# Performance work log

Hardware: AMD Instinct MI355X
Metric: run time of the kernel (lower is better)

## Reference

```python
import jax, jax.numpy as jnp
import numpy as np

EPS = 1e-5

def setup_inputs() -> dict:
    key = jax.random.key(0)
    ks = jax.random.split(key, 6)
    N, E, C, H, L = 50000, 800000, 128, 128, 3
    x = jax.random.normal(ks[0], (N, C), dtype=jnp.float32)
    edge_index = jax.random.randint(ks[1], (2, E), 0, N, dtype=jnp.int64)
    # Xavier-ish scaled weights; layer 0 uses in=C=H so all layers stack uniformly.
    Wl = jax.random.normal(ks[2], (L, C, H), dtype=jnp.float32) / np.sqrt(C)
    Wr = jax.random.normal(ks[3], (L, C, H), dtype=jnp.float32) / np.sqrt(C)
    b = jnp.zeros((L, H), dtype=jnp.float32)
    gamma = jnp.ones((L, H), dtype=jnp.float32)
    beta = jnp.zeros((L, H), dtype=jnp.float32)
    return {"x": x, "edge_index": edge_index, "Wl": Wl, "Wr": Wr, "b": b,
            "gamma": gamma, "beta": beta}

def _sage_bn_relu(x, src, dst, Wl, Wr, b, gamma, beta):
    N = x.shape[0]
    # mean aggregation of source features into target nodes (PyG SAGEConv default)
    agg = jax.ops.segment_sum(x[src], dst, num_segments=N)          # [N, C]
    deg = jax.ops.segment_sum(jnp.ones_like(dst, dtype=x.dtype), dst, num_segments=N)
    mean_nbr = agg / jnp.maximum(deg, 1.0)[:, None]
    h = mean_nbr @ Wl + x @ Wr + b                                   # [N, H]
    # BatchNorm1d (training-mode batch statistics over nodes)
    mu = jnp.mean(h, axis=0)
    var = jnp.var(h, axis=0)
    h = gamma * (h - mu) * jax.lax.rsqrt(var + EPS) + beta
    return jax.nn.relu(h)  # dropout omitted (deterministic reference, p->0)

def reference(x, edge_index, Wl, Wr, b, gamma, beta):
    src, dst = edge_index[0], edge_index[1]
    h = x
    for l in range(Wl.shape[0]):
        h = _sage_bn_relu(h, src, dst, Wl[l], Wr[l], b[l], gamma[l], beta[l])
    return h
```

## Files before the change

kernel.cpp:

```cpp
#include <hip/hip_runtime.h>
#include <hip/hip_bf16.h>

#define BN_EPS 1e-5f
#define BCAP 16384

typedef unsigned short u16;
typedef unsigned int u32;
typedef __attribute__((ext_vector_type(8))) short bf16x8v;
typedef __attribute__((ext_vector_type(4))) float f32x4v;

__device__ __forceinline__ float bf2f(u16 u){
    union { u32 i; float f; } c; c.i = ((u32)u) << 16; return c.f;
}
__device__ __forceinline__ u16 f2bf(float f){
    union { float f; u32 i; } c; c.f = f;
    u32 x = c.i;
    u32 r = x + 0x7FFFu + ((x >> 16) & 1u);
    return (u16)(r >> 16);
}
__device__ __forceinline__ float lo16(u32 u){
    union { u32 i; float f; } c; c.i = u << 16; return c.f;
}
__device__ __forceinline__ float hi16(u32 u){
    union { u32 i; float f; } c; c.i = u & 0xFFFF0000u; return c.f;
}
__device__ __forceinline__ u32 pack2(float f0, float f1){
    return (u32)f2bf(f0) | ((u32)f2bf(f1) << 16);
}

__global__ void detect_k(const int* __restrict__ ei, const u16* __restrict__ xu,
                         int* __restrict__ flags){
    int lane = threadIdx.x;
    unsigned long long bal = __ballot(ei[2 * lane + 1] != 0);
    int cnt = 0;
    #pragma unroll
    for (int k = 0; k < 4; ++k){
        u16 u = xu[2 * (lane + 64 * k)];
        int e = (u >> 7) & 0xFF;
        cnt += (e >= 0x70 && e <= 0x86) ? 1 : 0;
    }
    #pragma unroll
    for (int off = 1; off < 64; off <<= 1) cnt += __shfl_xor(cnt, off);
    if (lane == 0){
        flags[0] = (bal == 0ULL) ? 1 : 0;
        flags[1] = (cnt >= 128) ? 1 : 0;
    }
}

__global__ void prep_k(const void* __restrict__ x, const void* __restrict__ Wl,
                       const void* __restrict__ Wr, const void* __restrict__ b,
                       const void* __restrict__ g, const void* __restrict__ be,
                       u16* __restrict__ xb, u16* __restrict__ wT, float* __restrict__ p,
                       int total4, int wtot, int per, const int* __restrict__ flags){
    int i = blockIdx.x * blockDim.x + threadIdx.x;
    int bf = flags[1];
    if (i < total4){
        if (bf){
            ((uint2*)xb)[i] = ((const uint2*)x)[i];
        } else {
            float4 v = ((const float4*)x)[i];
            ushort4 o; o.x = f2bf(v.x); o.y = f2bf(v.y); o.z = f2bf(v.z); o.w = f2bf(v.w);
            ((ushort4*)xb)[i] = o;
        }
    }
    if (i < wtot){
        u16 vl = bf ? ((const u16*)Wl)[i] : f2bf(((const float*)Wl)[i]);
        u16 vr = bf ? ((const u16*)Wr)[i] : f2bf(((const float*)Wr)[i]);
        int l = i >> 14, r = (i >> 7) & 127, c = i & 127;
        wT[(size_t)(l * 2 + 0) * 16384 + c * 128 + r] = vl;
        wT[(size_t)(l * 2 + 1) * 16384 + c * 128 + r] = vr;
    }
    if (i < per){
        if (bf){
            p[i]           = bf2f(((const u16*)b)[i]);
            p[per + i]     = bf2f(((const u16*)g)[i]);
            p[2 * per + i] = bf2f(((const u16*)be)[i]);
        } else {
            p[i]           = ((const float*)b)[i];
            p[per + i]     = ((const float*)g)[i];
            p[2 * per + i] = ((const float*)be)[i];
        }
    }
}

__global__ __launch_bounds__(1024) void phist_k(const void* __restrict__ ei, int E,
                                                int tile, u32* __restrict__ blockHist,
                                                const int* __restrict__ flags){
    __shared__ u32 lh[128];
    int tid = threadIdx.x;
    if (tid < 128) lh[tid] = 0u;
    __syncthreads();
    int start = blockIdx.x * tile;
    int end = min(E, start + tile);
    int i64 = flags[0];
    for (int i = start + tid; i < end; i += 1024){
        int d = i64 ? (int)((const long long*)ei)[E + i] : ((const int*)ei)[E + i];
        atomicAdd(&lh[d >> 9], 1u);
    }
    __syncthreads();
    if (tid < 128) blockHist[blockIdx.x * 128 + tid] = lh[tid];
}

__global__ void bases_k(const u32* __restrict__ blockHist, u32* __restrict__ blockBase,
                        int* __restrict__ rangeBase, int* __restrict__ rowptrN, int nb){
    __shared__ u32 t_s[128];
    int k = threadIdx.x;
    u32 run = 0;
    for (int b = 0; b < nb; ++b){
        blockBase[b * 128 + k] = run;
        run += blockHist[b * 128 + k];
    }
    t_s[k] = min(run, (u32)BCAP);
    __syncthreads();
    if (k == 0){
        u32 r = 0;
        for (int j = 0; j < 128; ++j){ u32 v = t_s[j]; t_s[j] = r; r += v; }
        rangeBase[128] = (int)r;
        *rowptrN = (int)r;
    }
    __syncthreads();
    rangeBase[k] = (int)t_s[k];
}

__global__ __launch_bounds__(1024) void pscat_k(const void* __restrict__ ei, int E,
                                                int tile, const u32* __restrict__ blockBase,
                                                u32* __restrict__ part,
                                                const int* __restrict__ flags){
    __shared__ u32 lcur[128];
    int tid = threadIdx.x;
    if (tid < 128) lcur[tid] = blockBase[blockIdx.x * 128 + tid];
    __syncthreads();
    int start = blockIdx.x * tile;
    int end = min(E, start + tile);
    int i64 = flags[0];
    for (int i = start + tid; i < end; i += 1024){
        int s, d;
        if (i64){
            const long long* p = (const long long*)ei;
            s = (int)p[i]; d = (int)p[E + i];
        } else {
            const int* p = (const int*)ei;
            s = p[i]; d = p[E + i];
        }
        int k = d >> 9;
        u32 pos = atomicAdd(&lcur[k], 1u);
        if (pos < BCAP) part[(size_t)k * BCAP + pos] = (u32)(u16)s | ((u32)(d & 511) << 16);
    }
}

__global__ __launch_bounds__(1024) void build_k(const u32* __restrict__ part,
                                                const int* __restrict__ rangeBase,
                                                int* __restrict__ rowptr,
                                                float* __restrict__ dinv,
                                                u16* __restrict__ col, int N){
    __shared__ u32 bins[512];
    __shared__ u32 wsum[8];
    __shared__ u16 sorted[BCAP];
    int k   = blockIdx.x;
    int tid = threadIdx.x;
    int base = rangeBase[k];
    int cntk = rangeBase[k + 1] - base;
    int d0   = k << 9;
    if (tid < 512) bins[tid] = 0u;
    __syncthreads();
    const u32* pk = part + (size_t)k * BCAP;
    for (int i = tid; i < cntk; i += 1024)
        atomicAdd(&bins[pk[i] >> 16], 1u);
    __syncthreads();
    int lane = tid & 63, w = tid >> 6;
    u32 v = (tid < 512) ? bins[tid] : 0u;
    u32 sc = v;
    #pragma unroll
    for (int off = 1; off < 64; off <<= 1){
        u32 u = __shfl_up(sc, off);
        if (lane >= off) sc += u;
    }
    if (lane == 63 && w < 8) wsum[w] = sc;
    __syncthreads();
    if (tid == 0){
        u32 r = 0;
        #pragma unroll
        for (int j = 0; j < 8; ++j){ u32 t = wsum[j]; wsum[j] = r; r += t; }
    }
    __syncthreads();
    u32 excl = (w < 8 ? wsum[w] : 0u) + sc - v;
    if (tid < 512){
        int d = d0 + tid;
        if (d < N){
            rowptr[d] = base + (int)excl;
            dinv[d] = 1.f / fmaxf((float)v, 1.f);
        }
        bins[tid] = excl;
    }
    __syncthreads();
    for (int i = tid; i < cntk; i += 1024){
        u32 e = pk[i];
        u32 pos = atomicAdd(&bins[e >> 16], 1u);
        sorted[pos] = (u16)e;
    }
    __syncthreads();
    for (int i = tid; i < cntk; i += 1024)
        col[base + i] = sorted[i];
}

__global__ void agg_k(const u16* __restrict__ h, const int* __restrict__ rowptr,
                      const u16* __restrict__ col, const float* __restrict__ dinv,
                      u16* __restrict__ meanb, int N){
    int wid  = (blockIdx.x * blockDim.x + threadIdx.x) >> 6;
    int lane = threadIdx.x & 63;
    if (wid >= N) return;
    int q   = lane >> 4;
    int sub = lane & 15;
    int s = rowptr[wid], e = rowptr[wid + 1];
    float a[8] = {0.f,0.f,0.f,0.f,0.f,0.f,0.f,0.f};
    int i = s + q;
    for (; i + 4 < e; i += 8){
        int sn0 = col[i], sn1 = col[i + 4];
        uint4 v0 = *(const uint4*)(h + (size_t)sn0 * 128 + sub * 8);
        uint4 v1 = *(const uint4*)(h + (size_t)sn1 * 128 + sub * 8);
        a[0] += lo16(v0.x) + lo16(v1.x); a[1] += hi16(v0.x) + hi16(v1.x);
        a[2] += lo16(v0.y) + lo16(v1.y); a[3] += hi16(v0.y) + hi16(v1.y);
        a[4] += lo16(v0.z) + lo16(v1.z); a[5] += hi16(v0.z) + hi16(v1.z);
        a[6] += lo16(v0.w) + lo16(v1.w); a[7] += hi16(v0.w) + hi16(v1.w);
    }
    if (i < e){
        int sn = col[i];
        uint4 v = *(const uint4*)(h + (size_t)sn * 128 + sub * 8);
        a[0] += lo16(v.x); a[1] += hi16(v.x);
        a[2] += lo16(v.y); a[3] += hi16(v.y);
        a[4] += lo16(v.z); a[5] += hi16(v.z);
        a[6] += lo16(v.w); a[7] += hi16(v.w);
    }
    #pragma unroll
    for (int off = 16; off < 64; off <<= 1){
        #pragma unroll
        for (int j = 0; j < 8; ++j) a[j] += __shfl_xor(a[j], off);
    }
    if (q == 0){
        float di = dinv[wid];
        uint4 o;
        o.x = pack2(a[0] * di, a[1] * di);
        o.y = pack2(a[2] * di, a[3] * di);
        o.z = pack2(a[4] * di, a[5] * di);
        o.w = pack2(a[6] * di, a[7] * di);
        *(uint4*)(meanb + (size_t)wid * 128 + sub * 8) = o;
    }
}

__global__ __launch_bounds__(256) void gemm_k(
        const u16* __restrict__ Aa, const u16* __restrict__ Ab,
        const u16* __restrict__ wT, const float* __restrict__ bias,
        u16* __restrict__ hp16, float* __restrict__ stats, int N){
    __shared__ float s_stat[256];
    int tid  = threadIdx.x;
    int lane = tid & 63;
    int w    = tid >> 6;
    int wid  = blockIdx.x * 4 + w;
    int hl   = lane & 15;
    int quad = lane >> 4;
    int m0   = wid * 32;
    s_stat[tid] = 0.f;
    __syncthreads();

    f32x4v acc[2][8];
    #pragma unroll
    for (int r2 = 0; r2 < 2; ++r2)
        #pragma unroll
        for (int t = 0; t < 8; ++t) acc[r2][t] = (f32x4v){0.f, 0.f, 0.f, 0.f};

    if (m0 < N){
        const u16* arow0[2];
        const u16* arow1[2];
        #pragma unroll
        for (int r2 = 0; r2 < 2; ++r2){
            int rb = m0 + r2 * 16;
            if (rb + 16 > N) rb = N - 16;
            arow0[r2] = Aa + (size_t)(rb + hl) * 128 + quad * 8;
            arow1[r2] = Ab + (size_t)(rb + hl) * 128 + quad * 8;
        }
        #pragma unroll
        for (int half = 0; half < 2; ++half){
            const u16* A0 = half ? arow1[0] : arow0[0];
            const u16* A1 = half ? arow1[1] : arow0[1];
            const u16* Bp = wT + half * 16384 + (size_t)hl * 128 + quad * 8;
            #pragma unroll
            for (int kc = 0; kc < 128; kc += 32){
                bf16x8v af0 = *(const bf16x8v*)(A0 + kc);
                bf16x8v af1 = *(const bf16x8v*)(A1 + kc);
                #pragma unroll
                for (int t = 0; t < 8; ++t){
                    bf16x8v bf = *(const bf16x8v*)(Bp + t * 2048 + kc);
                    acc[0][t] = __builtin_amdgcn_mfma_f32_16x16x32_bf16(af0, bf, acc[0][t], 0, 0, 0);
                    acc[1][t] = __builtin_amdgcn_mfma_f32_16x16x32_bf16(af1, bf, acc[1][t], 0, 0, 0);
                }
            }
        }
    }

    #pragma unroll
    for (int r2 = 0; r2 < 2; ++r2){
        int mb = m0 + r2 * 16;
        bool valid = (mb < N);
        #pragma unroll
        for (int t = 0; t < 8; ++t){
            int c = t * 16 + hl;
            float bv = bias[c];
            float cs = 0.f, cq = 0.f;
            if (valid){
                #pragma unroll
                for (int r = 0; r < 4; ++r){
                    float v = acc[r2][t][r] + bv;
                    hp16[(size_t)(mb + quad * 4 + r) * 128 + c] = f2bf(v);
                    cs += v; cq += v * v;
                }
            }
            cs += __shfl_xor(cs, 16); cs += __shfl_xor(cs, 32);
            cq += __shfl_xor(cq, 16); cq += __shfl_xor(cq, 32);
            if (quad == 0 && valid){
                atomicAdd(&s_stat[c], cs);
                atomicAdd(&s_stat[128 + c], cq);
            }
        }
    }
    __syncthreads();
    float* st = stats + (size_t)(blockIdx.x & 63) * 256;
    atomicAdd(&st[tid], s_stat[tid]);
}

__global__ void finalize_k(float* __restrict__ stats, const float* __restrict__ g,
                           const float* __restrict__ be, float* __restrict__ ss, float invN){
    int j = threadIdx.x;
    float s = 0.f, sq = 0.f;
    #pragma unroll 8
    for (int bkt = 0; bkt < 64; ++bkt){
        s  += stats[bkt * 256 + j];
        sq += stats[bkt * 256 + 128 + j];
        stats[bkt * 256 + j] = 0.f;
        stats[bkt * 256 + 128 + j] = 0.f;
    }
    float mu  = s * invN;
    float var = sq * invN - mu * mu;
    if (!(mu == mu)) mu = 0.f;
    if (!(var >= 0.f) || !(var == var)) var = 0.f;
    float sc = g[j] * rsqrtf(var + BN_EPS);
    ss[j]       = sc;
    ss[128 + j] = be[j] - mu * sc;
}

__global__ void apply_k(const u16* __restrict__ in, const float* __restrict__ ss,
                        u16* __restrict__ outb, float* __restrict__ outf, int use_f32,
                        int total4){
    int i = blockIdx.x * blockDim.x + threadIdx.x;
    if (i >= total4) return;
    uint2 u = ((const uint2*)in)[i];
    float4 v;
    v.x = lo16(u.x); v.y = hi16(u.x); v.z = lo16(u.y); v.w = hi16(u.y);
    if (!(v.x == v.x)) v.x = 0.f;
    if (!(v.y == v.y)) v.y = 0.f;
    if (!(v.z == v.z)) v.z = 0.f;
    if (!(v.w == v.w)) v.w = 0.f;
    int c = (i & 31) * 4;
    float r0 = fmaxf(v.x * ss[c]     + ss[128 + c], 0.f);
    float r1 = fmaxf(v.y * ss[c + 1] + ss[129 + c], 0.f);
    float r2 = fmaxf(v.z * ss[c + 2] + ss[130 + c], 0.f);
    float r3 = fmaxf(v.w * ss[c + 3] + ss[131 + c], 0.f);
    if (use_f32){
        float4 o; o.x = r0; o.y = r1; o.z = r2; o.w = r3;
        ((float4*)outf)[i] = o;
    } else {
        uint2 o; o.x = pack2(r0, r1); o.y = pack2(r2, r3);
        ((uint2*)outb)[i] = o;
    }
}

extern "C" void kernel_launch(void* const* d_in, const int* in_sizes, int n_in,
                              void* d_out, int out_size, void* d_ws, size_t ws_size,
                              hipStream_t stream){
    const void* x  = d_in[0];
    const int*  ei = (const int*)d_in[1];
    const void* Wl = d_in[2];
    const void* Wr = d_in[3];
    const void* b  = d_in[4];
    const void* gm = d_in[5];
    const void* bt = d_in[6];
    float* outf = (float*)d_out;

    const int N = in_sizes[0] / 128;
    const int E = in_sizes[1] / 2;
    const int L = in_sizes[2] / 16384;
    const int PB = 128;
    const int TILE = (E + PB - 1) / PB;

    char* wsp = (char*)d_ws;
    size_t off = 0;
    auto alloc = [&](size_t bytes) -> char* {
        char* p = wsp + off;
        off = (off + bytes + 255) & ~(size_t)255;
        return p;
    };
    int*   flags  = (int*)  alloc(16);
    int*   rowptr = (int*)  alloc((size_t)(N + 1) * 4);
    u16*   col    = (u16*)  alloc((size_t)E * 2);
    float* dinv   = (float*)alloc((size_t)N * 4);
    u32*   bHist  = (u32*)  alloc((size_t)PB * 128 * 4);
    u32*   bBase  = (u32*)  alloc((size_t)PB * 128 * 4);
    int*   rangeB = (int*)  alloc((size_t)129 * 4);
    u32*   part   = (u32*)  alloc((size_t)128 * BCAP * 4);
    u16*   wT     = (u16*)  alloc((size_t)L * 2 * 16384 * 2);
    float* pvec   = (float*)alloc((size_t)3 * L * 128 * 4);
    float* ss     = (float*)alloc(256 * 4);
    u16*   xb     = (u16*)  alloc((size_t)N * 128 * 2);
    u16*   meanb  = (u16*)  alloc((size_t)N * 128 * 2);
    float* stats  = (float*)alloc((size_t)64 * 256 * 4);
    u16*   hpre16 = (u16*)  alloc((size_t)N * 128 * 2);
    u16*   hA     = (u16*)  alloc((size_t)N * 128 * 2);
    u16*   hB     = (u16*)  alloc((size_t)N * 128 * 2);
    (void)ws_size; (void)n_in; (void)out_size;

    detect_k<<<1, 64, 0, stream>>>(ei, (const u16*)x, flags);
    hipMemsetAsync(stats, 0, (size_t)64 * 256 * 4, stream);

    phist_k<<<PB, 1024, 0, stream>>>((const void*)ei, E, TILE, bHist, flags);
    bases_k<<<1, 128, 0, stream>>>(bHist, bBase, rangeB, rowptr + N, PB);
    pscat_k<<<PB, 1024, 0, stream>>>((const void*)ei, E, TILE, bBase, part, flags);
    build_k<<<128, 1024, 0, stream>>>(part, rangeB, rowptr, dinv, col, N);

    prep_k<<<(N * 32 + 255) / 256, 256, 0, stream>>>(x, Wl, Wr, b, gm, bt, xb, wT, pvec,
                                                     N * 32, L * 16384, L * 128, flags);

    const u16* state = xb;
    int nwaves = (N + 31) / 32;
    int gblocks = (nwaves + 3) / 4;
    for (int l = 0; l < L; ++l){
        int last = (l == L - 1);
        u16* nxt = (l & 1) ? hB : hA;
        agg_k<<<(N + 3) / 4, 256, 0, stream>>>(state, rowptr, col, dinv, meanb, N);
        gemm_k<<<gblocks, 256, 0, stream>>>(meanb, state, wT + (size_t)l * 2 * 16384,
                                            pvec + l * 128, hpre16, stats, N);
        finalize_k<<<1, 128, 0, stream>>>(stats, pvec + (size_t)L * 128 + l * 128,
                                          pvec + (size_t)2 * L * 128 + l * 128,
                                          ss, 1.f / (float)N);
        apply_k<<<(N * 32 + 255) / 256, 256, 0, stream>>>(hpre16, ss, nxt, outf, last,
                                                          N * 32);
        state = nxt;
    }
}
```

Before: 350.4 us.

## Fuse GEMM, BatchNorm finalize and apply via in-kernel grid barrier

The GEMM kernel now keeps its pre-norm outputs in registers, accumulates batch statistics, and waits on a software grid-wide barrier. After the barrier every block computes the scale and shift and writes the normalized ReLU output directly. This removes the finalize and apply launches and the bf16 round trip of the intermediate activation. The catch is that it depends on all 196 blocks of 512 threads being resident at once, and it contends on a single global stats array instead of 64 buckets; the spin loop has a timeout that would silently give wrong results if residency fails.

After: 394.5 us. 1.13x slower.

```diff
diff --git a/kernel.cpp b/kernel.cpp
--- a/kernel.cpp
+++ b/kernel.cpp
@@ -247,19 +247,23 @@
     }
 }
 
-__global__ __launch_bounds__(256) void gemm_k(
+__global__ __launch_bounds__(512, 2) void gemm_k(
         const u16* __restrict__ Aa, const u16* __restrict__ Ab,
         const u16* __restrict__ wT, const float* __restrict__ bias,
-        u16* __restrict__ hp16, float* __restrict__ stats, int N){
+        const float* __restrict__ gamma, const float* __restrict__ beta,
+        float* __restrict__ stats, u32* __restrict__ bar,
+        u16* __restrict__ outb, float* __restrict__ outf,
+        int use_f32, int N, float invN){
     __shared__ float s_stat[256];
+    __shared__ float s_ss[256];
     int tid  = threadIdx.x;
     int lane = tid & 63;
     int w    = tid >> 6;
-    int wid  = blockIdx.x * 4 + w;
+    int wid  = blockIdx.x * 8 + w;
     int hl   = lane & 15;
     int quad = lane >> 4;
     int m0   = wid * 32;
-    s_stat[tid] = 0.f;
+    if (tid < 256) s_stat[tid] = 0.f;
     __syncthreads();
 
     f32x4v acc[2][8];
@@ -295,81 +299,85 @@
                 }
             }
         }
-    }
-
-    #pragma unroll
-    for (int r2 = 0; r2 < 2; ++r2){
-        int mb = m0 + r2 * 16;
-        bool valid = (mb < N);
-        #pragma unroll
-        for (int t = 0; t < 8; ++t){
-            int c = t * 16 + hl;
-            float bv = bias[c];
-            float cs = 0.f, cq = 0.f;
-            if (valid){
+
+        #pragma unroll
+        for (int r2 = 0; r2 < 2; ++r2){
+            int mb = m0 + r2 * 16;
+            bool valid = (mb < N);
+            #pragma unroll
+            for (int t = 0; t < 8; ++t){
+                int c = t * 16 + hl;
+                float bv = bias[c];
+                float cs = 0.f, cq = 0.f;
                 #pragma unroll
                 for (int r = 0; r < 4; ++r){
                     float v = acc[r2][t][r] + bv;
-                    hp16[(size_t)(mb + quad * 4 + r) * 128 + c] = f2bf(v);
+                    acc[r2][t][r] = v;
                     cs += v; cq += v * v;
                 }
+                cs += __shfl_xor(cs, 16); cs += __shfl_xor(cs, 32);
+                cq += __shfl_xor(cq, 16); cq += __shfl_xor(cq, 32);
+                if (quad == 0 && valid){
+                    atomicAdd(&s_stat[c], cs);
+                    atomicAdd(&s_stat[128 + c], cq);
+                }
             }
-            cs += __shfl_xor(cs, 16); cs += __shfl_xor(cs, 32);
-            cq += __shfl_xor(cq, 16); cq += __shfl_xor(cq, 32);
-            if (quad == 0 && valid){
-                atomicAdd(&s_stat[c], cs);
-                atomicAdd(&s_stat[128 + c], cq);
+        }
+    }
+    __syncthreads();
+    if (tid < 256) atomicAdd(&stats[tid], s_stat[tid]);
+
+    __syncthreads();
+    if (tid == 0){
+        __threadfence();
+        u32 nb = gridDim.x;
+        u32 my = __hip_atomic_load(&bar[1], __ATOMIC_RELAXED, __HIP_MEMORY_SCOPE_AGENT);
+        u32 old = __hip_atomic_fetch_add(&bar[0], 1u, __ATOMIC_ACQ_REL, __HIP_MEMORY_SCOPE_AGENT);
+        if (old == nb - 1){
+            __hip_atomic_store(&bar[0], 0u, __ATOMIC_RELAXED, __HIP_MEMORY_SCOPE_AGENT);
+            __hip_atomic_fetch_add(&bar[1], 1u, __ATOMIC_RELEASE, __HIP_MEMORY_SCOPE_AGENT);
+        } else {
+            int spins = 0;
+            while (__hip_atomic_load(&bar[1], __ATOMIC_ACQUIRE, __HIP_MEMORY_SCOPE_AGENT) == my){
+                __builtin_amdgcn_s_sleep(2);
+                if (++spins > 20000000) break;
             }
         }
     }
     __syncthreads();
-    float* st = stats + (size_t)(blockIdx.x & 63) * 256;
-    atomicAdd(&st[tid], s_stat[tid]);
-}
-
-__global__ void finalize_k(float* __restrict__ stats, const float* __restrict__ g,
-                           const float* __restrict__ be, float* __restrict__ ss, float invN){
-    int j = threadIdx.x;
-    float s = 0.f, sq = 0.f;
-    #pragma unroll 8
-    for (int bkt = 0; bkt < 64; ++bkt){
-        s  += stats[bkt * 256 + j];
-        sq += stats[bkt * 256 + 128 + j];
-        stats[bkt * 256 + j] = 0.f;
-        stats[bkt * 256 + 128 + j] = 0.f;
-    }
-    float mu  = s * invN;
-    float var = sq * invN - mu * mu;
-    if (!(mu == mu)) mu = 0.f;
-    if (!(var >= 0.f) || !(var == var)) var = 0.f;
-    float sc = g[j] * rsqrtf(var + BN_EPS);
-    ss[j]       = sc;
-    ss[128 + j] = be[j] - mu * sc;
-}
-
-__global__ void apply_k(const u16* __restrict__ in, const float* __restrict__ ss,
-                        u16* __restrict__ outb, float* __restrict__ outf, int use_f32,
-                        int total4){
-    int i = blockIdx.x * blockDim.x + threadIdx.x;
-    if (i >= total4) return;
-    uint2 u = ((const uint2*)in)[i];
-    float4 v;
-    v.x = lo16(u.x); v.y = hi16(u.x); v.z = lo16(u.y); v.w = hi16(u.y);
-    if (!(v.x == v.x)) v.x = 0.f;
-    if (!(v.y == v.y)) v.y = 0.f;
-    if (!(v.z == v.z)) v.z = 0.f;
-    if (!(v.w == v.w)) v.w = 0.f;
-    int c = (i & 31) * 4;
-    float r0 = fmaxf(v.x * ss[c]     + ss[128 + c], 0.f);
-    float r1 = fmaxf(v.y * ss[c + 1] + ss[129 + c], 0.f);
-    float r2 = fmaxf(v.z * ss[c + 2] + ss[130 + c], 0.f);
-    float r3 = fmaxf(v.w * ss[c + 3] + ss[131 + c], 0.f);
-    if (use_f32){
-        float4 o; o.x = r0; o.y = r1; o.z = r2; o.w = r3;
-        ((float4*)outf)[i] = o;
-    } else {
-        uint2 o; o.x = pack2(r0, r1); o.y = pack2(r2, r3);
-        ((uint2*)outb)[i] = o;
+
+    if (tid < 128){
+        float s  = __hip_atomic_load(&stats[tid],       __ATOMIC_RELAXED, __HIP_MEMORY_SCOPE_AGENT);
+        float sq = __hip_atomic_load(&stats[128 + tid], __ATOMIC_RELAXED, __HIP_MEMORY_SCOPE_AGENT);
+        float mu  = s * invN;
+        float var = sq * invN - mu * mu;
+        if (!(mu == mu)) mu = 0.f;
+        if (!(var >= 0.f) || !(var == var)) var = 0.f;
+        float sc = gamma[tid] * rsqrtf(var + BN_EPS);
+        s_ss[tid]       = sc;
+        s_ss[128 + tid] = beta[tid] - mu * sc;
+    }
+    __syncthreads();
+
+    if (m0 < N){
+        #pragma unroll
+        for (int r2 = 0; r2 < 2; ++r2){
+            int mb = m0 + r2 * 16;
+            if (mb >= N) continue;
+            #pragma unroll
+            for (int t = 0; t < 8; ++t){
+                int c = t * 16 + hl;
+                float sc = s_ss[c];
+                float sh = s_ss[128 + c];
+                #pragma unroll
+                for (int r = 0; r < 4; ++r){
+                    float y = fmaxf(acc[r2][t][r] * sc + sh, 0.f);
+                    size_t idx = (size_t)(mb + quad * 4 + r) * 128 + c;
+                    if (use_f32) outf[idx] = y;
+                    else         outb[idx] = f2bf(y);
+                }
+            }
+        }
     }
 }
 
@@ -408,17 +416,16 @@
     u32*   part   = (u32*)  alloc((size_t)128 * BCAP * 4);
     u16*   wT     = (u16*)  alloc((size_t)L * 2 * 16384 * 2);
     float* pvec   = (float*)alloc((size_t)3 * L * 128 * 4);
-    float* ss     = (float*)alloc(256 * 4);
+    u32*   bar    = (u32*)  alloc(256);
+    float* stats  = (float*)alloc((size_t)L * 256 * 4);
     u16*   xb     = (u16*)  alloc((size_t)N * 128 * 2);
     u16*   meanb  = (u16*)  alloc((size_t)N * 128 * 2);
-    float* stats  = (float*)alloc((size_t)64 * 256 * 4);
-    u16*   hpre16 = (u16*)  alloc((size_t)N * 128 * 2);
     u16*   hA     = (u16*)  alloc((size_t)N * 128 * 2);
     u16*   hB     = (u16*)  alloc((size_t)N * 128 * 2);
     (void)ws_size; (void)n_in; (void)out_size;
 
     detect_k<<<1, 64, 0, stream>>>(ei, (const u16*)x, flags);
-    hipMemsetAsync(stats, 0, (size_t)64 * 256 * 4, stream);
+    hipMemsetAsync(bar, 0, 256 + (size_t)L * 256 * 4, stream);
 
     phist_k<<<PB, 1024, 0, stream>>>((const void*)ei, E, TILE, bHist, flags);
     bases_k<<<1, 128, 0, stream>>>(bHist, bBase, rangeB, rowptr + N, PB);
@@ -429,19 +436,19 @@
                                                      N * 32, L * 16384, L * 128, flags);
 
     const u16* state = xb;
-    int nwaves = (N + 31) / 32;
-    int gblocks = (nwaves + 3) / 4;
+    int nwaves  = (N + 31) / 32;
+    int gblocks = (nwaves + 7) / 8;
+    float invN  = 1.f / (float)N;
     for (int l = 0; l < L; ++l){
         int last = (l == L - 1);
         u16* nxt = (l & 1) ? hB : hA;
         agg_k<<<(N + 3) / 4, 256, 0, stream>>>(state, rowptr, col, dinv, meanb, N);
-        gemm_k<<<gblocks, 256, 0, stream>>>(meanb, state, wT + (size_t)l * 2 * 16384,
-                                            pvec + l * 128, hpre16, stats, N);
-        finalize_k<<<1, 128, 0, stream>>>(stats, pvec + (size_t)L * 128 + l * 128,
-                                          pvec + (size_t)2 * L * 128 + l * 128,
-                                          ss, 1.f / (float)N);
-        apply_k<<<(N * 32 + 255) / 256, 256, 0, stream>>>(hpre16, ss, nxt, outf, last,
-                                                          N * 32);
+        gemm_k<<<gblocks, 512, 0, stream>>>(meanb, state, wT + (size_t)l * 2 * 16384,
+                                            pvec + (size_t)l * 128,
+                                            pvec + (size_t)L * 128 + (size_t)l * 128,
+                                            pvec + (size_t)2 * L * 128 + (size_t)l * 128,
+                                            stats + (size_t)l * 256, bar,
+                                            nxt, outf, last, N, invN);
         state = nxt;
     }
 }
```

## Fold BatchNorm+ReLU of previous layer into next layer's aggregation and GEMM loads

Applied to the files above, without the earlier changes.

Drops the per-layer apply pass. The raw pre-activation output of each layer is stored as the state, and the previous layer's BN scale/shift plus ReLU are applied on the fly. This happens when neighbor features are gathered in agg_k and when the self features are loaded in gemm_k. A single apply_k runs only at the end to write the fp32 output. The GEMM also moves from 32 to 16 rows per wave. Per-layer stats buffers remove the zeroing inside finalize. Each edge gather now pays an extra FMA and max per element, and the GEMM does per-element bf16 conversion on the self operand; in exchange, two full-tensor passes per layer go away.

Result: slower. 383.4 us (+9.4%).

```diff
diff --git a/kernel.cpp b/kernel.cpp
--- a/kernel.cpp
+++ b/kernel.cpp
@@ -51,6 +51,7 @@
                        const void* __restrict__ Wr, const void* __restrict__ b,
                        const void* __restrict__ g, const void* __restrict__ be,
                        u16* __restrict__ xb, u16* __restrict__ wT, float* __restrict__ p,
+                       float* __restrict__ ssAll,
                        int total4, int wtot, int per, const int* __restrict__ flags){
     int i = blockIdx.x * blockDim.x + threadIdx.x;
     int bf = flags[1];
@@ -80,6 +81,10 @@
             p[per + i]     = ((const float*)g)[i];
             p[2 * per + i] = ((const float*)be)[i];
         }
+    }
+    if (i < 128){
+        ssAll[i]       = 1.f;
+        ssAll[128 + i] = 0.f;
     }
 }
 
@@ -205,32 +210,45 @@
 
 __global__ void agg_k(const u16* __restrict__ h, const int* __restrict__ rowptr,
                       const u16* __restrict__ col, const float* __restrict__ dinv,
-                      u16* __restrict__ meanb, int N){
+                      const float* __restrict__ ss, u16* __restrict__ meanb,
+                      float reluLo, int N){
     int wid  = (blockIdx.x * blockDim.x + threadIdx.x) >> 6;
     int lane = threadIdx.x & 63;
     if (wid >= N) return;
     int q   = lane >> 4;
     int sub = lane & 15;
+    float scr[8], shr[8];
+    #pragma unroll
+    for (int j = 0; j < 8; ++j){
+        scr[j] = ss[sub * 8 + j];
+        shr[j] = ss[128 + sub * 8 + j];
+    }
     int s = rowptr[wid], e = rowptr[wid + 1];
     float a[8] = {0.f,0.f,0.f,0.f,0.f,0.f,0.f,0.f};
     int i = s + q;
+    #define BNR(x, j) fmaxf((x) * scr[j] + shr[j], reluLo)
     for (; i + 4 < e; i += 8){
         int sn0 = col[i], sn1 = col[i + 4];
         uint4 v0 = *(const uint4*)(h + (size_t)sn0 * 128 + sub * 8);
         uint4 v1 = *(const uint4*)(h + (size_t)sn1 * 128 + sub * 8);
-        a[0] += lo16(v0.x) + lo16(v1.x); a[1] += hi16(v0.x) + hi16(v1.x);
-        a[2] += lo16(v0.y) + lo16(v1.y); a[3] += hi16(v0.y) + hi16(v1.y);
-        a[4] += lo16(v0.z) + lo16(v1.z); a[5] += hi16(v0.z) + hi16(v1.z);
-        a[6] += lo16(v0.w) + lo16(v1.w); a[7] += hi16(v0.w) + hi16(v1.w);
+        a[0] += BNR(lo16(v0.x),0) + BNR(lo16(v1.x),0);
+        a[1] += BNR(hi16(v0.x),1) + BNR(hi16(v1.x),1);
+        a[2] += BNR(lo16(v0.y),2) + BNR(lo16(v1.y),2);
+        a[3] += BNR(hi16(v0.y),3) + BNR(hi16(v1.y),3);
+        a[4] += BNR(lo16(v0.z),4) + BNR(lo16(v1.z),4);
+        a[5] += BNR(hi16(v0.z),5) + BNR(hi16(v1.z),5);
+        a[6] += BNR(lo16(v0.w),6) + BNR(lo16(v1.w),6);
+        a[7] += BNR(hi16(v0.w),7) + BNR(hi16(v1.w),7);
     }
     if (i < e){
         int sn = col[i];
         uint4 v = *(const uint4*)(h + (size_t)sn * 128 + sub * 8);
-        a[0] += lo16(v.x); a[1] += hi16(v.x);
-        a[2] += lo16(v.y); a[3] += hi16(v.y);
-        a[4] += lo16(v.z); a[5] += hi16(v.z);
-        a[6] += lo16(v.w); a[7] += hi16(v.w);
-    }
+        a[0] += BNR(lo16(v.x),0); a[1] += BNR(hi16(v.x),1);
+        a[2] += BNR(lo16(v.y),2); a[3] += BNR(hi16(v.y),3);
+        a[4] += BNR(lo16(v.z),4); a[5] += BNR(hi16(v.z),5);
+        a[6] += BNR(lo16(v.w),6); a[7] += BNR(hi16(v.w),7);
+    }
+    #undef BNR
     #pragma unroll
     for (int off = 16; off < 64; off <<= 1){
         #pragma unroll
@@ -250,73 +268,74 @@
 __global__ __launch_bounds__(256) void gemm_k(
         const u16* __restrict__ Aa, const u16* __restrict__ Ab,
         const u16* __restrict__ wT, const float* __restrict__ bias,
-        u16* __restrict__ hp16, float* __restrict__ stats, int N){
+        const float* __restrict__ ssPrev, float* __restrict__ stats,
+        u16* __restrict__ hp16, float reluLo, int N){
     __shared__ float s_stat[256];
+    __shared__ float s_ss[256];
     int tid  = threadIdx.x;
     int lane = tid & 63;
     int w    = tid >> 6;
     int wid  = blockIdx.x * 4 + w;
     int hl   = lane & 15;
     int quad = lane >> 4;
-    int m0   = wid * 32;
+    int m0   = wid * 16;
     s_stat[tid] = 0.f;
-    __syncthreads();
-
-    f32x4v acc[2][8];
-    #pragma unroll
-    for (int r2 = 0; r2 < 2; ++r2)
+    s_ss[tid]   = ssPrev[tid];
+    __syncthreads();
+
+    f32x4v acc[8];
+    #pragma unroll
+    for (int t = 0; t < 8; ++t) acc[t] = (f32x4v){0.f, 0.f, 0.f, 0.f};
+
+    if (m0 < N){
+        int rb = m0;
+        if (rb + 16 > N) rb = N - 16;
+        const u16* a0 = Aa + (size_t)(rb + hl) * 128 + quad * 8;
+        const u16* a1 = Ab + (size_t)(rb + hl) * 128 + quad * 8;
+
         #pragma unroll
-        for (int t = 0; t < 8; ++t) acc[r2][t] = (f32x4v){0.f, 0.f, 0.f, 0.f};
-
-    if (m0 < N){
-        const u16* arow0[2];
-        const u16* arow1[2];
+        for (int kc = 0; kc < 128; kc += 32){
+            bf16x8v af = *(const bf16x8v*)(a0 + kc);
+            const u16* Bp = wT + (size_t)hl * 128 + quad * 8 + kc;
+            #pragma unroll
+            for (int t = 0; t < 8; ++t){
+                bf16x8v bf = *(const bf16x8v*)(Bp + t * 2048);
+                acc[t] = __builtin_amdgcn_mfma_f32_16x16x32_bf16(af, bf, acc[t], 0, 0, 0);
+            }
+        }
         #pragma unroll
-        for (int r2 = 0; r2 < 2; ++r2){
-            int rb = m0 + r2 * 16;
-            if (rb + 16 > N) rb = N - 16;
-            arow0[r2] = Aa + (size_t)(rb + hl) * 128 + quad * 8;
-            arow1[r2] = Ab + (size_t)(rb + hl) * 128 + quad * 8;
-        }
-        #pragma unroll
-        for (int half = 0; half < 2; ++half){
-            const u16* A0 = half ? arow1[0] : arow0[0];
-            const u16* A1 = half ? arow1[1] : arow0[1];
-            const u16* Bp = wT + half * 16384 + (size_t)hl * 128 + quad * 8;
+        for (int kc = 0; kc < 128; kc += 32){
+            bf16x8v raw = *(const bf16x8v*)(a1 + kc);
+            bf16x8v af;
             #pragma unroll
-            for (int kc = 0; kc < 128; kc += 32){
-                bf16x8v af0 = *(const bf16x8v*)(A0 + kc);
-                bf16x8v af1 = *(const bf16x8v*)(A1 + kc);
-                #pragma unroll
-                for (int t = 0; t < 8; ++t){
-                    bf16x8v bf = *(const bf16x8v*)(Bp + t * 2048 + kc);
-                    acc[0][t] = __builtin_amdgcn_mfma_f32_16x16x32_bf16(af0, bf, acc[0][t], 0, 0, 0);
-                    acc[1][t] = __builtin_amdgcn_mfma_f32_16x16x32_bf16(af1, bf, acc[1][t], 0, 0, 0);
-                }
+            for (int j = 0; j < 8; ++j){
+                int c = quad * 8 + kc + j;
+                float f = bf2f((u16)raw[j]);
+                f = fmaxf(f * s_ss[c] + s_ss[128 + c], reluLo);
+                af[j] = (short)f2bf(f);
             }
-        }
-    }
-
-    #pragma unroll
-    for (int r2 = 0; r2 < 2; ++r2){
-        int mb = m0 + r2 * 16;
-        bool valid = (mb < N);
+            const u16* Bp = wT + 16384 + (size_t)hl * 128 + quad * 8 + kc;
+            #pragma unroll
+            for (int t = 0; t < 8; ++t){
+                bf16x8v bf = *(const bf16x8v*)(Bp + t * 2048);
+                acc[t] = __builtin_amdgcn_mfma_f32_16x16x32_bf16(af, bf, acc[t], 0, 0, 0);
+            }
+        }
+
         #pragma unroll
         for (int t = 0; t < 8; ++t){
             int c = t * 16 + hl;
             float bv = bias[c];
             float cs = 0.f, cq = 0.f;
-            if (valid){
-                #pragma unroll
-                for (int r = 0; r < 4; ++r){
-                    float v = acc[r2][t][r] + bv;
-                    hp16[(size_t)(mb + quad * 4 + r) * 128 + c] = f2bf(v);
-                    cs += v; cq += v * v;
-                }
+            #pragma unroll
+            for (int r = 0; r < 4; ++r){
+                float v = acc[t][r] + bv;
+                hp16[(size_t)(rb + quad * 4 + r) * 128 + c] = f2bf(v);
+                cs += v; cq += v * v;
             }
             cs += __shfl_xor(cs, 16); cs += __shfl_xor(cs, 32);
             cq += __shfl_xor(cq, 16); cq += __shfl_xor(cq, 32);
-            if (quad == 0 && valid){
+            if (quad == 0){
                 atomicAdd(&s_stat[c], cs);
                 atomicAdd(&s_stat[128 + c], cq);
             }
@@ -327,29 +346,27 @@
     atomicAdd(&st[tid], s_stat[tid]);
 }
 
-__global__ void finalize_k(float* __restrict__ stats, const float* __restrict__ g,
-                           const float* __restrict__ be, float* __restrict__ ss, float invN){
+__global__ void finalize_k(const float* __restrict__ stats, const float* __restrict__ g,
+                           const float* __restrict__ be, float* __restrict__ ssOut,
+                           float invN){
     int j = threadIdx.x;
     float s = 0.f, sq = 0.f;
     #pragma unroll 8
     for (int bkt = 0; bkt < 64; ++bkt){
         s  += stats[bkt * 256 + j];
         sq += stats[bkt * 256 + 128 + j];
-        stats[bkt * 256 + j] = 0.f;
-        stats[bkt * 256 + 128 + j] = 0.f;
     }
     float mu  = s * invN;
     float var = sq * invN - mu * mu;
     if (!(mu == mu)) mu = 0.f;
     if (!(var >= 0.f) || !(var == var)) var = 0.f;
     float sc = g[j] * rsqrtf(var + BN_EPS);
-    ss[j]       = sc;
-    ss[128 + j] = be[j] - mu * sc;
+    ssOut[j]       = sc;
+    ssOut[128 + j] = be[j] - mu * sc;
 }
 
 __global__ void apply_k(const u16* __restrict__ in, const float* __restrict__ ss,
-                        u16* __restrict__ outb, float* __restrict__ outf, int use_f32,
-                        int total4){
+                        float* __restrict__ outf, int total4){
     int i = blockIdx.x * blockDim.x + threadIdx.x;
     if (i >= total4) return;
     uint2 u = ((const uint2*)in)[i];
@@ -360,17 +377,12 @@
     if (!(v.z == v.z)) v.z = 0.f;
     if (!(v.w == v.w)) v.w = 0.f;
     int c = (i & 31) * 4;
-    float r0 = fmaxf(v.x * ss[c]     + ss[128 + c], 0.f);
-    float r1 = fmaxf(v.y * ss[c + 1] + ss[129 + c], 0.f);
-    float r2 = fmaxf(v.z * ss[c + 2] + ss[130 + c], 0.f);
-    float r3 = fmaxf(v.w * ss[c + 3] + ss[131 + c], 0.f);
-    if (use_f32){
-        float4 o; o.x = r0; o.y = r1; o.z = r2; o.w = r3;
-        ((float4*)outf)[i] = o;
-    } else {
-        uint2 o; o.x = pack2(r0, r1); o.y = pack2(r2, r3);
-        ((uint2*)outb)[i] = o;
-    }
+    float4 o;
+    o.x = fmaxf(v.x * ss[c]     + ss[128 + c], 0.f);
+    o.y = fmaxf(v.y * ss[c + 1] + ss[129 + c], 0.f);
+    o.z = fmaxf(v.z * ss[c + 2] + ss[130 + c], 0.f);
+    o.w = fmaxf(v.w * ss[c + 3] + ss[131 + c], 0.f);
+    ((float4*)outf)[i] = o;
 }
 
 extern "C" void kernel_launch(void* const* d_in, const int* in_sizes, int n_in,
@@ -408,17 +420,16 @@
     u32*   part   = (u32*)  alloc((size_t)128 * BCAP * 4);
     u16*   wT     = (u16*)  alloc((size_t)L * 2 * 16384 * 2);
     float* pvec   = (float*)alloc((size_t)3 * L * 128 * 4);
-    float* ss     = (float*)alloc(256 * 4);
+    float* ssAll  = (float*)alloc((size_t)(L + 1) * 256 * 4);
+    float* stats  = (float*)alloc((size_t)L * 64 * 256 * 4);
     u16*   xb     = (u16*)  alloc((size_t)N * 128 * 2);
     u16*   meanb  = (u16*)  alloc((size_t)N * 128 * 2);
-    float* stats  = (float*)alloc((size_t)64 * 256 * 4);
-    u16*   hpre16 = (u16*)  alloc((size_t)N * 128 * 2);
     u16*   hA     = (u16*)  alloc((size_t)N * 128 * 2);
     u16*   hB     = (u16*)  alloc((size_t)N * 128 * 2);
     (void)ws_size; (void)n_in; (void)out_size;
 
     detect_k<<<1, 64, 0, stream>>>(ei, (const u16*)x, flags);
-    hipMemsetAsync(stats, 0, (size_t)64 * 256 * 4, stream);
+    hipMemsetAsync(stats, 0, (size_t)L * 64 * 256 * 4, stream);
 
     phist_k<<<PB, 1024, 0, stream>>>((const void*)ei, E, TILE, bHist, flags);
     bases_k<<<1, 128, 0, stream>>>(bHist, bBase, rangeB, rowptr + N, PB);
@@ -426,22 +437,29 @@
     build_k<<<128, 1024, 0, stream>>>(part, rangeB, rowptr, dinv, col, N);
 
     prep_k<<<(N * 32 + 255) / 256, 256, 0, stream>>>(x, Wl, Wr, b, gm, bt, xb, wT, pvec,
-                                                     N * 32, L * 16384, L * 128, flags);
+                                                     ssAll, N * 32, L * 16384, L * 128,
+                                                     flags);
 
     const u16* state = xb;
-    int nwaves = (N + 31) / 32;
+    int nwaves  = (N + 15) / 16;
     int gblocks = (nwaves + 3) / 4;
+    float invN  = 1.f / (float)N;
     for (int l = 0; l < L; ++l){
-        int last = (l == L - 1);
         u16* nxt = (l & 1) ? hB : hA;
-        agg_k<<<(N + 3) / 4, 256, 0, stream>>>(state, rowptr, col, dinv, meanb, N);
+        float reluLo = (l == 0) ? -3.0e38f : 0.f;
+        agg_k<<<(N + 3) / 4, 256, 0, stream>>>(state, rowptr, col, dinv,
+                                               ssAll + (size_t)l * 256, meanb, reluLo, N);
         gemm_k<<<gblocks, 256, 0, stream>>>(meanb, state, wT + (size_t)l * 2 * 16384,
-                                            pvec + l * 128, hpre16, stats, N);
-        finalize_k<<<1, 128, 0, stream>>>(stats, pvec + (size_t)L * 128 + l * 128,
-                                          pvec + (size_t)2 * L * 128 + l * 128,
-                                          ss, 1.f / (float)N);
-        apply_k<<<(N * 32 + 255) / 256, 256, 0, stream>>>(hpre16, ss, nxt, outf, last,
-                                                          N * 32);
+                                            pvec + (size_t)l * 128,
+                                            ssAll + (size_t)l * 256,
+                                            stats + (size_t)l * 64 * 256,
+                                            nxt, reluLo, N);
+        finalize_k<<<1, 128, 0, stream>>>(stats + (size_t)l * 64 * 256,
+                                          pvec + (size_t)L * 128 + (size_t)l * 128,
+                                          pvec + (size_t)2 * L * 128 + (size_t)l * 128,
+                                          ssAll + (size_t)(l + 1) * 256, invN);
         state = nxt;
     }
-}
+    apply_k<<<(N * 32 + 255) / 256, 256, 0, stream>>>(state, ssAll + (size_t)L * 256,
+                                                      outf, N * 32);
+}
```

## Keep weight fragments in registers with a persistent per-wave column split in GEMM

Applied to the files above, without the earlier changes.

The GEMM now gives each wave a fixed 32-column slice of the output. Each wave loads its weight fragments into registers once, and the block loops over row tiles across a reduced grid. BatchNorm sums are accumulated in registers across tiles and flushed with a few global atomics, which removes the shared-memory stats and block barriers. Stats buffers are now per layer and zeroed once up front, so finalize no longer clears them. In exchange, every wave re-reads the same A rows and register pressure goes up.

After: 343.2 us. 2.1% less time.

```diff
diff --git a/kernel.cpp b/kernel.cpp
--- a/kernel.cpp
+++ b/kernel.cpp
@@ -250,93 +250,111 @@
 __global__ __launch_bounds__(256) void gemm_k(
         const u16* __restrict__ Aa, const u16* __restrict__ Ab,
         const u16* __restrict__ wT, const float* __restrict__ bias,
-        u16* __restrict__ hp16, float* __restrict__ stats, int N){
-    __shared__ float s_stat[256];
+        float* __restrict__ stats, u16* __restrict__ hp16, int N, int NT){
     int tid  = threadIdx.x;
     int lane = tid & 63;
     int w    = tid >> 6;
-    int wid  = blockIdx.x * 4 + w;
     int hl   = lane & 15;
     int quad = lane >> 4;
-    int m0   = wid * 32;
-    s_stat[tid] = 0.f;
-    __syncthreads();
-
-    f32x4v acc[2][8];
-    #pragma unroll
-    for (int r2 = 0; r2 < 2; ++r2)
-        #pragma unroll
-        for (int t = 0; t < 8; ++t) acc[r2][t] = (f32x4v){0.f, 0.f, 0.f, 0.f};
-
-    if (m0 < N){
-        const u16* arow0[2];
-        const u16* arow1[2];
-        #pragma unroll
-        for (int r2 = 0; r2 < 2; ++r2){
-            int rb = m0 + r2 * 16;
-            if (rb + 16 > N) rb = N - 16;
-            arow0[r2] = Aa + (size_t)(rb + hl) * 128 + quad * 8;
-            arow1[r2] = Ab + (size_t)(rb + hl) * 128 + quad * 8;
-        }
-        #pragma unroll
-        for (int half = 0; half < 2; ++half){
-            const u16* A0 = half ? arow1[0] : arow0[0];
-            const u16* A1 = half ? arow1[1] : arow0[1];
-            const u16* Bp = wT + half * 16384 + (size_t)hl * 128 + quad * 8;
+    int c0   = (2 * w)     * 16 + hl;
+    int c1   = (2 * w + 1) * 16 + hl;
+
+    bf16x8v Bf[2][2][4];
+    {
+        const u16* bp = wT + (size_t)(2 * w) * 2048 + (size_t)hl * 128 + quad * 8;
+        #pragma unroll
+        for (int tl = 0; tl < 2; ++tl)
             #pragma unroll
-            for (int kc = 0; kc < 128; kc += 32){
-                bf16x8v af0 = *(const bf16x8v*)(A0 + kc);
-                bf16x8v af1 = *(const bf16x8v*)(A1 + kc);
+            for (int half = 0; half < 2; ++half)
                 #pragma unroll
-                for (int t = 0; t < 8; ++t){
-                    bf16x8v bf = *(const bf16x8v*)(Bp + t * 2048 + kc);
-                    acc[0][t] = __builtin_amdgcn_mfma_f32_16x16x32_bf16(af0, bf, acc[0][t], 0, 0, 0);
-                    acc[1][t] = __builtin_amdgcn_mfma_f32_16x16x32_bf16(af1, bf, acc[1][t], 0, 0, 0);
+                for (int kc = 0; kc < 4; ++kc)
+                    Bf[tl][half][kc] =
+                        *(const bf16x8v*)(bp + tl * 2048 + half * 16384 + kc * 32);
+    }
+    float bv0 = bias[c0], bv1 = bias[c1];
+    float cs0 = 0.f, cq0 = 0.f, cs1 = 0.f, cq1 = 0.f;
+
+    for (int tile = blockIdx.x; tile < NT; tile += gridDim.x){
+        int m0  = tile * 32;
+        int rb0 = m0;      bool v0 = (rb0 + 16 <= N); if (!v0) rb0 = N - 16;
+        int rb1 = m0 + 16; bool v1 = (rb1 + 16 <= N); if (!v1) rb1 = N - 16;
+        const u16* paa0 = Aa + (size_t)(rb0 + hl) * 128 + quad * 8;
+        const u16* pab0 = Ab + (size_t)(rb0 + hl) * 128 + quad * 8;
+        const u16* paa1 = Aa + (size_t)(rb1 + hl) * 128 + quad * 8;
+        const u16* pab1 = Ab + (size_t)(rb1 + hl) * 128 + quad * 8;
+
+        bf16x8v A0[2][4], A1[2][4];
+        #pragma unroll
+        for (int kc = 0; kc < 4; ++kc){
+            A0[0][kc] = *(const bf16x8v*)(paa0 + kc * 32);
+            A1[0][kc] = *(const bf16x8v*)(paa1 + kc * 32);
+            A0[1][kc] = *(const bf16x8v*)(pab0 + kc * 32);
+            A1[1][kc] = *(const bf16x8v*)(pab1 + kc * 32);
+        }
+
+        f32x4v acc0[2], acc1[2];
+        #pragma unroll
+        for (int tl = 0; tl < 2; ++tl){
+            acc0[tl] = (f32x4v){0.f, 0.f, 0.f, 0.f};
+            acc1[tl] = (f32x4v){0.f, 0.f, 0.f, 0.f};
+        }
+        #pragma unroll
+        for (int half = 0; half < 2; ++half)
+            #pragma unroll
+            for (int kc = 0; kc < 4; ++kc)
+                #pragma unroll
+                for (int tl = 0; tl < 2; ++tl){
+                    acc0[tl] = __builtin_amdgcn_mfma_f32_16x16x32_bf16(
+                        A0[half][kc], Bf[tl][half][kc], acc0[tl], 0, 0, 0);
+                    acc1[tl] = __builtin_amdgcn_mfma_f32_16x16x32_bf16(
+                        A1[half][kc], Bf[tl][half][kc], acc1[tl], 0, 0, 0);
+                }
+
+        #pragma unroll
+        for (int tl = 0; tl < 2; ++tl){
+            int   c  = tl ? c1 : c0;
+            float bv = tl ? bv1 : bv0;
+            if (v0){
+                #pragma unroll
+                for (int r = 0; r < 4; ++r){
+                    float v = acc0[tl][r] + bv;
+                    hp16[(size_t)(rb0 + quad * 4 + r) * 128 + c] = f2bf(v);
+                    if (tl){ cs1 += v; cq1 += v * v; } else { cs0 += v; cq0 += v * v; }
                 }
             }
-        }
-    }
-
-    #pragma unroll
-    for (int r2 = 0; r2 < 2; ++r2){
-        int mb = m0 + r2 * 16;
-        bool valid = (mb < N);
-        #pragma unroll
-        for (int t = 0; t < 8; ++t){
-            int c = t * 16 + hl;
-            float bv = bias[c];
-            float cs = 0.f, cq = 0.f;
-            if (valid){
+            if (v1){
                 #pragma unroll
                 for (int r = 0; r < 4; ++r){
-                    float v = acc[r2][t][r] + bv;
-                    hp16[(size_t)(mb + quad * 4 + r) * 128 + c] = f2bf(v);
-                    cs += v; cq += v * v;
+                    float v = acc1[tl][r] + bv;
+                    hp16[(size_t)(rb1 + quad * 4 + r) * 128 + c] = f2bf(v);
+                    if (tl){ cs1 += v; cq1 += v * v; } else { cs0 += v; cq0 += v * v; }
                 }
             }
-            cs += __shfl_xor(cs, 16); cs += __shfl_xor(cs, 32);
-            cq += __shfl_xor(cq, 16); cq += __shfl_xor(cq, 32);
-            if (quad == 0 && valid){
-                atomicAdd(&s_stat[c], cs);
-                atomicAdd(&s_stat[128 + c], cq);
-            }
-        }
-    }
-    __syncthreads();
-    float* st = stats + (size_t)(blockIdx.x & 63) * 256;
-    atomicAdd(&st[tid], s_stat[tid]);
-}
-
-__global__ void finalize_k(float* __restrict__ stats, const float* __restrict__ g,
-                           const float* __restrict__ be, float* __restrict__ ss, float invN){
+        }
+    }
+
+    cs0 += __shfl_xor(cs0, 16); cs0 += __shfl_xor(cs0, 32);
+    cq0 += __shfl_xor(cq0, 16); cq0 += __shfl_xor(cq0, 32);
+    cs1 += __shfl_xor(cs1, 16); cs1 += __shfl_xor(cs1, 32);
+    cq1 += __shfl_xor(cq1, 16); cq1 += __shfl_xor(cq1, 32);
+    if (quad == 0){
+        float* st = stats + (size_t)(blockIdx.x & 63) * 256;
+        atomicAdd(&st[c0],       cs0);
+        atomicAdd(&st[128 + c0], cq0);
+        atomicAdd(&st[c1],       cs1);
+        atomicAdd(&st[128 + c1], cq1);
+    }
+}
+
+__global__ void finalize_k(const float* __restrict__ stats, const float* __restrict__ g,
+                           const float* __restrict__ be, float* __restrict__ ss,
+                           float invN){
     int j = threadIdx.x;
     float s = 0.f, sq = 0.f;
     #pragma unroll 8
     for (int bkt = 0; bkt < 64; ++bkt){
         s  += stats[bkt * 256 + j];
         sq += stats[bkt * 256 + 128 + j];
-        stats[bkt * 256 + j] = 0.f;
-        stats[bkt * 256 + 128 + j] = 0.f;
     }
     float mu  = s * invN;
     float var = sq * invN - mu * mu;
@@ -409,16 +427,16 @@
     u16*   wT     = (u16*)  alloc((size_t)L * 2 * 16384 * 2);
     float* pvec   = (float*)alloc((size_t)3 * L * 128 * 4);
     float* ss     = (float*)alloc(256 * 4);
+    float* stats  = (float*)alloc((size_t)L * 64 * 256 * 4);
     u16*   xb     = (u16*)  alloc((size_t)N * 128 * 2);
     u16*   meanb  = (u16*)  alloc((size_t)N * 128 * 2);
-    float* stats  = (float*)alloc((size_t)64 * 256 * 4);
     u16*   hpre16 = (u16*)  alloc((size_t)N * 128 * 2);
     u16*   hA     = (u16*)  alloc((size_t)N * 128 * 2);
     u16*   hB     = (u16*)  alloc((size_t)N * 128 * 2);
     (void)ws_size; (void)n_in; (void)out_size;
 
     detect_k<<<1, 64, 0, stream>>>(ei, (const u16*)x, flags);
-    hipMemsetAsync(stats, 0, (size_t)64 * 256 * 4, stream);
+    hipMemsetAsync(stats, 0, (size_t)L * 64 * 256 * 4, stream);
 
     phist_k<<<PB, 1024, 0, stream>>>((const void*)ei, E, TILE, bHist, flags);
     bases_k<<<1, 128, 0, stream>>>(bHist, bBase, rangeB, rowptr + N, PB);
@@ -429,17 +447,21 @@
                                                      N * 32, L * 16384, L * 128, flags);
 
     const u16* state = xb;
-    int nwaves = (N + 31) / 32;
-    int gblocks = (nwaves + 3) / 4;
+    int NT      = (N + 31) / 32;
+    int gblocks = (NT + 2) / 3;
+    float invN  = 1.f / (float)N;
     for (int l = 0; l < L; ++l){
         int last = (l == L - 1);
         u16* nxt = (l & 1) ? hB : hA;
         agg_k<<<(N + 3) / 4, 256, 0, stream>>>(state, rowptr, col, dinv, meanb, N);
         gemm_k<<<gblocks, 256, 0, stream>>>(meanb, state, wT + (size_t)l * 2 * 16384,
-                                            pvec + l * 128, hpre16, stats, N);
-        finalize_k<<<1, 128, 0, stream>>>(stats, pvec + (size_t)L * 128 + l * 128,
+                                            pvec + (size_t)l * 128,
+                                            stats + (size_t)l * 64 * 256,
+                                            hpre16, N, NT);
+        finalize_k<<<1, 128, 0, stream>>>(stats + (size_t)l * 64 * 256,
+                                          pvec + (size_t)L * 128 + l * 128,
                                           pvec + (size_t)2 * L * 128 + l * 128,
-                                          ss, 1.f / (float)N);
+                                          ss, invN);
         apply_k<<<(N * 32 + 255) / 256, 256, 0, stream>>>(hpre16, ss, nxt, outf, last,
                                                           N * 32);
         state = nxt;
```
